# Performance work log

Hardware: AMD Instinct MI355X
Metric: run time of the kernel (lower is better)

The kernel has to match this reference:

```python
import jax, jax.numpy as jnp
import numpy as np

N = 50000
E = 1600000
INPUT_DIM = 128
HEADS = 4
OUT_DIM = 32
LRELU_ALPHA = 0.2


def setup_inputs() -> dict:
    key = jax.random.key(0)
    k1, k2, k3, k4, k5 = jax.random.split(key, 5)
    gain = 1.0 / (1.0 + LRELU_ALPHA)
    input_proj = jax.random.normal(k1, (N, INPUT_DIM), dtype=jnp.float32)
    edge_index = jax.random.randint(k2, (2, E), 0, N, dtype=jnp.int64)
    W = jax.random.normal(k3, (INPUT_DIM, HEADS * OUT_DIM), dtype=jnp.float32) * (gain / INPUT_DIM) ** 0.5
    A_left = jax.random.normal(k4, (HEADS, OUT_DIM, 1), dtype=jnp.float32) * (gain / OUT_DIM)
    A_right = jax.random.normal(k5, (HEADS, OUT_DIM, 1), dtype=jnp.float32) * (gain / OUT_DIM)
    return {"input_proj": input_proj, "edge_index": edge_index, "W": W, "A_left": A_left, "A_right": A_right}


def reference(input_proj, edge_index, W, A_left, A_right):
    n = input_proj.shape[0]
    heads, out_dim = A_left.shape[0], A_left.shape[1]
    # Linear projection: [N, heads, out_dim]
    H = (input_proj @ W).reshape(n, heads, out_dim)
    # Per-node attention scores: [N, heads]
    H_s = jnp.einsum('nhd,hd->nh', H, A_left[..., 0])
    H_t = jnp.einsum('nhd,hd->nh', H, A_right[..., 0])
    src = edge_index[0]
    tgt = edge_index[1]
    # Edge scores: leaky_relu(H_s[src] + H_t[tgt]) -> [E, heads]
    e = H_s[src] + H_t[tgt]
    e = jnp.where(e > 0, e, LRELU_ALPHA * e)
    # Segment softmax over neighborhoods keyed by source node (global max shift, as in original)
    e = jnp.exp(e - jnp.max(e))
    denom = jax.ops.segment_sum(e, src, num_segments=n)  # [N, heads]
    alpha = e / (denom[src] + 1e-8)
    # Weighted scatter-add aggregation of target features: [N, heads, out_dim]
    msg = alpha[:, :, None] * H[tgt]
    agg = jax.ops.segment_sum(msg, src, num_segments=n)
    # concat_last=True -> [N, heads*out_dim], then ELU
    res = agg.reshape(n, heads * out_dim)
    return jax.nn.elu(res)
```

## Files before the change

### kernel.cpp

```cpp
#include <hip/hip_runtime.h>
#include <hip/hip_fp16.h>

#define DIM 128
#define HEADS 4
#define ODIM 32
#define LRELU 0.2f
#define PT 4096
#define CAP 9216

typedef unsigned int u32;
typedef unsigned short u16;
typedef unsigned char u8;

typedef __attribute__((ext_vector_type(8))) short bf16x8;
typedef __attribute__((ext_vector_type(4))) float f32x4;

__device__ __forceinline__ u16 f2bf(float f) {
    union { u32 u; float f; } x; x.f = f;
    u32 u = x.u;
    u32 r = u + 0x7FFFu + ((u >> 16) & 1u);
    return (u16)(r >> 16);
}
__device__ __forceinline__ u32 pack_h2(float x, float y) {
    union { __half2 h; u32 u; } c;
    c.h = __floats2half2_rn(x, y);
    return c.u;
}
__device__ __forceinline__ float2 up2(u32 b) {
    union { u32 u; __half2 h; } c; c.u = b;
    return __half22float2(c.h);
}

__device__ __forceinline__ int scan256_excl(int v, int t, int* wsum) {
    int lane = t & 63, w = t >> 6;
    int inc = v;
    #pragma unroll
    for (int ofs = 1; ofs < 64; ofs <<= 1) {
        int x = __shfl_up(inc, ofs);
        if (lane >= ofs) inc += x;
    }
    __syncthreads();
    if (lane == 63) wsum[w] = inc;
    __syncthreads();
    int add = 0;
    #pragma unroll
    for (int j = 0; j < 4; ++j) add += (j < w) ? wsum[j] : 0;
    return inc - v + add;
}

__global__ __launch_bounds__(256) void prep_kernel(
    const float* __restrict__ W, u16* __restrict__ Wt, int* __restrict__ bcur)
{
    __shared__ u16 s[128 * 17];
    const int t = threadIdx.x;
    const int b = blockIdx.x;
    if (b == 0) bcur[t] = t * CAP;
    #pragma unroll
    for (int i = 0; i < 8; ++i) {
        int idx = i * 256 + t;
        int kk = idx >> 7;
        int nn = idx & 127;
        s[nn * 17 + kk] = f2bf(W[(b * 16 + kk) * 128 + nn]);
    }
    __syncthreads();
    #pragma unroll
    for (int i = 0; i < 8; ++i) {
        int idx = i * 256 + t;
        int nn = idx >> 4;
        int kk = idx & 15;
        Wt[nn * 128 + b * 16 + kk] = s[nn * 17 + kk];
    }
}

__device__ __forceinline__ void partition_body(
    char* smem, int bid, const int* __restrict__ ei, int* __restrict__ bcur,
    u32* __restrict__ part, int E, int n)
{
    u32* stage = (u32*)smem;
    u8*  sbkt  = (u8*)(smem + 16384);
    int (*lcnt4)[256] = (int (*)[256])(smem + 20480);
    int (*lcur4)[256] = (int (*)[256])(smem + 24576);
    int* loff  = (int*)(smem + 28672);
    int* ltot  = (int*)(smem + 29696);
    int* gbase = (int*)(smem + 30720);
    int* wsum  = (int*)(smem + 31744);
    const int t = threadIdx.x;
    const int wv = t >> 6;
    const int base = bid * PT;
    lcnt4[0][t] = 0; lcnt4[1][t] = 0; lcnt4[2][t] = 0; lcnt4[3][t] = 0;
    __syncthreads();

    int srcv[16], tgtv[16];
    #pragma unroll
    for (int i = 0; i < 16; ++i) {
        int e = base + i * 256 + t;
        srcv[i] = (e < E) ? ei[e] : -1;
    }
    #pragma unroll
    for (int i = 0; i < 16; ++i) {
        int e = base + i * 256 + t;
        tgtv[i] = (e < E) ? ei[E + e] : 0;
    }
    u32 key[16];
    int bkt[16];
    #pragma unroll
    for (int i = 0; i < 16; ++i) {
        bkt[i] = -1;
        key[i] = 0;
        if (srcv[i] >= 0) {
            int src = min(srcv[i], n - 1);
            int tgt = max(0, min(tgtv[i], n - 1));
            bkt[i] = src >> 8;
            key[i] = ((u32)(src & 255) << 17) | (u32)tgt;
        }
    }
    #pragma unroll
    for (int i = 0; i < 16; ++i)
        if (bkt[i] >= 0) atomicAdd(&lcnt4[wv][bkt[i]], 1);
    __syncthreads();
    int c0 = lcnt4[0][t], c1 = lcnt4[1][t], c2 = lcnt4[2][t], c3 = lcnt4[3][t];
    int total = c0 + c1 + c2 + c3;
    int ex = scan256_excl(total, t, wsum);
    loff[t] = ex;
    ltot[t] = total;
    lcur4[0][t] = ex;
    lcur4[1][t] = ex + c0;
    lcur4[2][t] = ex + c0 + c1;
    lcur4[3][t] = ex + c0 + c1 + c2;
    gbase[t] = (total > 0) ? atomicAdd(&bcur[t], total) : 0;
    __syncthreads();
    #pragma unroll
    for (int i = 0; i < 16; ++i) {
        if (bkt[i] >= 0) {
            int p = atomicAdd(&lcur4[wv][bkt[i]], 1);
            stage[p] = key[i];
            sbkt[p] = (u8)bkt[i];
        }
    }
    __syncthreads();
    int tot = loff[255] + ltot[255];
    for (int i = t; i < tot; i += 256) {
        int b = sbkt[i];
        int dst = gbase[b] + (i - loff[b]);
        if (dst < (b + 1) * CAP) part[dst] = stage[i];
    }
}

__device__ __forceinline__ void proj_body(
    char* smem, int bid, const float* __restrict__ X, const u16* __restrict__ Wt,
    const float* __restrict__ AL, const float* __restrict__ AR,
    u32* __restrict__ Hb, float* __restrict__ Hs, float* __restrict__ Ht, int n)
{
    float* sH  = (float*)smem;
    float* sAL = (float*)(smem + 33792);
    float* sAR = (float*)(smem + 34304);
    const int t = threadIdx.x;
    if (t < DIM) { sAL[t] = AL[t]; sAR[t] = AR[t]; }
    const int row0 = bid * 64;
    const int w = t >> 6, lane = t & 63;
    const int quad = lane >> 4, nIdx = lane & 15;
    const int m = row0 + w * 16 + nIdx;

    f32x4 acc[8];
    #pragma unroll
    for (int c = 0; c < 8; ++c) acc[c] = (f32x4){0.f, 0.f, 0.f, 0.f};

    #pragma unroll
    for (int kq = 0; kq < 4; ++kq) {
        union { bf16x8 v; u16 e[8]; } a;
        if (m < n) {
            const float* xp = &X[(size_t)m * DIM + kq * 32 + quad * 8];
            float4 x0 = *(const float4*)xp;
            float4 x1 = *(const float4*)(xp + 4);
            a.e[0] = f2bf(x0.x); a.e[1] = f2bf(x0.y);
            a.e[2] = f2bf(x0.z); a.e[3] = f2bf(x0.w);
            a.e[4] = f2bf(x1.x); a.e[5] = f2bf(x1.y);
            a.e[6] = f2bf(x1.z); a.e[7] = f2bf(x1.w);
        } else {
            #pragma unroll
            for (int j = 0; j < 8; ++j) a.e[j] = 0;
        }
        #pragma unroll
        for (int c = 0; c < 8; ++c) {
            bf16x8 b = *(const bf16x8*)&Wt[(c * 16 + nIdx) * DIM + kq * 32 + quad * 8];
            acc[c] = __builtin_amdgcn_mfma_f32_16x16x32_bf16(a.v, b, acc[c], 0, 0, 0);
        }
    }
    #pragma unroll
    for (int c = 0; c < 8; ++c)
        #pragma unroll
        for (int r = 0; r < 4; ++r)
            sH[(w * 16 + quad * 4 + r) * 132 + c * 16 + nIdx] = acc[c][r];
    __syncthreads();

    #pragma unroll
    for (int i = 0; i < 16; ++i) {
        int idx = i * 256 + t;
        int r = idx >> 6, d2 = idx & 63;
        int gr = row0 + r;
        if (gr < n) {
            float2 hv = *(const float2*)&sH[r * 132 + 2 * d2];
            Hb[(size_t)gr * 64 + d2] = pack_h2(hv.x, hv.y);
        }
    }
    {
        int r = t >> 2, h = t & 3;
        float s = 0.f, s2 = 0.f;
        #pragma unroll
        for (int q = 0; q < ODIM; q += 4) {
            float4 hv = *(const float4*)&sH[r * 132 + h * ODIM + q];
            s  += hv.x*sAL[h*ODIM+q] + hv.y*sAL[h*ODIM+q+1] + hv.z*sAL[h*ODIM+q+2] + hv.w*sAL[h*ODIM+q+3];
            s2 += hv.x*sAR[h*ODIM+q] + hv.y*sAR[h*ODIM+q+1] + hv.z*sAR[h*ODIM+q+2] + hv.w*sAR[h*ODIM+q+3];
        }
        int gr = row0 + r;
        if (gr < n) { Hs[gr * HEADS + h] = s; Ht[gr * HEADS + h] = s2; }
    }
}

__global__ __launch_bounds__(256) void fused_pp_kernel(
    const float* __restrict__ X, const u16* __restrict__ Wt,
    const float* __restrict__ AL, const float* __restrict__ AR,
    u32* __restrict__ Hb, float* __restrict__ Hs, float* __restrict__ Ht,
    const int* __restrict__ ei, int* __restrict__ bcur, u32* __restrict__ part,
    int n, int E, int partBlocks)
{
    __shared__ alignas(16) char smem[34816];
    if ((int)blockIdx.x < partBlocks)
        partition_body(smem, blockIdx.x, ei, bcur, part, E, n);
    else
        proj_body(smem, blockIdx.x - partBlocks, X, Wt, AL, AR, Hb, Hs, Ht, n);
}

__global__ __launch_bounds__(256) void csrfill_kernel(
    const u32* __restrict__ part, const int* __restrict__ bcur,
    int* __restrict__ off, int* __restrict__ csr_tgt, int n, int ntiles)
{
    __shared__ u32 skey[CAP];
    __shared__ int lc4[4][128];
    __shared__ int lcur4[4][128];
    __shared__ int wsum[4];
    __shared__ int sBase, sCnt;
    const int blk = blockIdx.x, t = threadIdx.x;
    const int b = blk >> 1, half = blk & 1;
    const int wv = t >> 6;
    int myc = (t < ntiles) ? (bcur[t] - t * CAP) : 0;
    myc = max(0, min(myc, CAP));
    int ex = scan256_excl(myc, t, wsum);
    if (t == b) { sBase = ex; sCnt = myc; }
    if (t < 128) { lc4[0][t] = 0; lc4[1][t] = 0; lc4[2][t] = 0; lc4[3][t] = 0; }
    __syncthreads();
    const int pbase = b * CAP;
    const int base = sBase, cnt = sCnt;
    for (int i = t; i < cnt; i += 1024) {
        u32 k[4];
        #pragma unroll
        for (int u = 0; u < 4; ++u) {
            int idx = i + u * 256;
            k[u] = (idx < cnt) ? part[pbase + idx] : 0xFFFFFFFFu;
        }
        #pragma unroll
        for (int u = 0; u < 4; ++u) {
            int idx = i + u * 256;
            if (idx < cnt) skey[idx] = k[u];
            int n8 = (int)(k[u] >> 17);
            if ((n8 >> 7) == half) atomicAdd(&lc4[wv][n8 & 127], 1);
        }
    }
    __syncthreads();
    int c0 = 0, c1 = 0, c2 = 0, c3 = 0, total = 0;
    if (t < 128) {
        c0 = lc4[0][t]; c1 = lc4[1][t]; c2 = lc4[2][t]; c3 = lc4[3][t];
        total = c0 + c1 + c2 + c3;
    }
    int ex2 = scan256_excl(total, t, wsum);
    int halfTot = wsum[0] + wsum[1];
    int myBase = base + (half ? (cnt - halfTot) : 0);
    if (t < 128) {
        lcur4[0][t] = ex2;
        lcur4[1][t] = ex2 + c0;
        lcur4[2][t] = ex2 + c0 + c1;
        lcur4[3][t] = ex2 + c0 + c1 + c2;
        int node = b * 256 + half * 128 + t;
        if (node < n) off[node] = myBase + ex2;
    }
    if (b == ntiles - 1 && half == 0 && t == 0) off[n] = base + cnt;
    __syncthreads();
    for (int i = t; i < cnt; i += 256) {
        u32 key = skey[i];
        int n8 = (int)(key >> 17);
        if ((n8 >> 7) == half) {
            int p = atomicAdd(&lcur4[wv][n8 & 127], 1);
            csr_tgt[myBase + p] = (int)(key & 0x1FFFFu);
        }
    }
}

__global__ __launch_bounds__(256) void agg_kernel(
    const u32* __restrict__ Hb, const float* __restrict__ Hs,
    const float* __restrict__ Ht, const int* __restrict__ off,
    const int* __restrict__ csr_tgt, float2* __restrict__ out, int n, int E)
{
    int node = (blockIdx.x * 256 + threadIdx.x) >> 6;
    int L = threadIdx.x & 63;
    if (node >= n) return;
    int lo = off[node], hi = off[node + 1];
    lo = max(0, min(lo, E));
    hi = max(lo, min(hi, E));
    if (hi <= lo) {
        out[(size_t)node * 64 + L] = {0.f, 0.f};
        return;
    }
    const int h = L >> 4;
    const int jSel = L >> 2;
    const int hSel = L & 3;
    float4 hs4 = *(const float4*)&Hs[node * HEADS];
    float hsD = hSel == 0 ? hs4.x : hSel == 1 ? hs4.y : hSel == 2 ? hs4.z : hs4.w;
    float ax = 0.f, ay = 0.f, Sd = 0.f;

    int tl = csr_tgt[min(lo + (L & 31), hi - 1)];
    for (int i = lo; i < hi; i += 32) {
        int tln = 0;
        if (i + 32 < hi) tln = csr_tgt[min(i + 32 + (L & 31), hi - 1)];
        int tA = __shfl(tl, jSel);
        int tB = __shfl(tl, jSel + 16);
        float eA = hsD + Ht[tA * HEADS + hSel];
        float eB = hsD + Ht[tB * HEADS + hSel];
        float wA = (i + jSel < hi)
                       ? __expf(fminf(eA > 0.f ? eA : LRELU * eA, 30.f)) : 0.f;
        float wB = (i + jSel + 16 < hi)
                       ? __expf(fminf(eB > 0.f ? eB : LRELU * eB, 30.f)) : 0.f;
        Sd += wA + wB;
        u32 bb[32];
        #pragma unroll
        for (int j = 0; j < 32; ++j) {
            int sj = __builtin_amdgcn_readlane(tl, j);
            bb[j] = Hb[((size_t)(u32)sj << 6) + L];
        }
        #pragma unroll
        for (int j = 0; j < 16; ++j) {
            float wj = __shfl(wA, (j << 2) | h);
            float2 f = up2(bb[j]);
            ax += wj * f.x;
            ay += wj * f.y;
        }
        #pragma unroll
        for (int j = 0; j < 16; ++j) {
            float wj = __shfl(wB, (j << 2) | h);
            float2 f = up2(bb[j + 16]);
            ax += wj * f.x;
            ay += wj * f.y;
        }
        tl = tln;
    }
    float S = 0.f;
    #pragma unroll
    for (int j = 0; j < 16; ++j) S += __shfl(Sd, (j << 2) | h);
    float inv = 1.f / (S + 1e-8f);
    float ox = ax * inv, oy = ay * inv;
    ox = ox > 0.f ? ox : (__expf(ox) - 1.f);
    oy = oy > 0.f ? oy : (__expf(oy) - 1.f);
    out[(size_t)node * 64 + L] = {ox, oy};
}

extern "C" void kernel_launch(void* const* d_in, const int* in_sizes, int n_in,
                              void* d_out, int out_size, void* d_ws, size_t ws_size,
                              hipStream_t stream) {
    const float* X  = (const float*)d_in[0];
    const int*   EI = (const int*)d_in[1];
    const float* W  = (const float*)d_in[2];
    const float* AL = (const float*)d_in[3];
    const float* AR = (const float*)d_in[4];
    const int n = in_sizes[0] / DIM;
    const int E = in_sizes[1] / 2;
    const int ntiles = (n + 255) / 256;

    char* ws = (char*)d_ws;
    size_t o = 0;
    auto alloc = [&](size_t bytes) -> void* {
        o = (o + 255) & ~(size_t)255;
        void* p = ws + o;
        o += bytes;
        return p;
    };
    int*   bcur    = (int*)alloc(256 * 4);
    u16*   Wt      = (u16*)alloc((size_t)DIM * DIM * 2);
    int*   off     = (int*)alloc((size_t)(n + 1) * 4);
    float* Hs      = (float*)alloc((size_t)n * HEADS * 4);
    float* Ht      = (float*)alloc((size_t)n * HEADS * 4);
    int*   csr_tgt = (int*)alloc((size_t)E * 4);
    u32*   part    = (u32*)alloc((size_t)ntiles * CAP * 4);
    u32*   Hb      = (u32*)alloc((size_t)n * 64 * 4);

    const int PB = (E + PT - 1) / PT;
    const int JB = (n + 63) / 64;

    prep_kernel<<<8, 256, 0, stream>>>(W, Wt, bcur);
    fused_pp_kernel<<<PB + JB, 256, 0, stream>>>(
        X, Wt, AL, AR, Hb, Hs, Ht, EI, bcur, part, n, E, PB);
    csrfill_kernel<<<ntiles * 2, 256, 0, stream>>>(part, bcur, off, csr_tgt, n, ntiles);
    agg_kernel<<<(n + 3) / 4, 256, 0, stream>>>(
        Hb, Hs, Ht, off, csr_tgt, (float2*)d_out, n, E);
}
```

Measured before the change: 184.5 us.

## Regroup kernels: fuse W prep with partition, fuse CSR fill with projection

Moves the W transpose into the same launch as edge partitioning, and runs the CSR fill alongside the node projection, which no longer depends on partitioning. The bucket cursor is now zeroed with a memset and holds relative counts. The CSR fill drops its 36KB shared staging buffer and rereads the partition from global memory on its second pass, which lowers shared memory per block so more blocks fit and co-schedule with projection blocks. The intent is to remove one dependent launch and overlap the independent projection with the CSR build, at the cost of an extra global read of the partition and a memset call.

```diff
diff --git a/kernel.cpp b/kernel.cpp
--- a/kernel.cpp
+++ b/kernel.cpp
@@ -48,13 +48,11 @@
     return inc - v + add;
 }
 
-__global__ __launch_bounds__(256) void prep_kernel(
-    const float* __restrict__ W, u16* __restrict__ Wt, int* __restrict__ bcur)
-{
-    __shared__ u16 s[128 * 17];
+__device__ __forceinline__ void wtprep_body(
+    char* smem, int b, const float* __restrict__ W, u16* __restrict__ Wt)
+{
+    u16* s = (u16*)smem;
     const int t = threadIdx.x;
-    const int b = blockIdx.x;
-    if (b == 0) bcur[t] = t * CAP;
     #pragma unroll
     for (int i = 0; i < 8; ++i) {
         int idx = i * 256 + t;
@@ -127,7 +125,8 @@
     lcur4[1][t] = ex + c0;
     lcur4[2][t] = ex + c0 + c1;
     lcur4[3][t] = ex + c0 + c1 + c2;
-    gbase[t] = (total > 0) ? atomicAdd(&bcur[t], total) : 0;
+    int gb = (total > 0) ? atomicAdd(&bcur[t], total) : 0;
+    gbase[t] = t * CAP + gb;
     __syncthreads();
     #pragma unroll
     for (int i = 0; i < 16; ++i) {
@@ -143,6 +142,89 @@
         int b = sbkt[i];
         int dst = gbase[b] + (i - loff[b]);
         if (dst < (b + 1) * CAP) part[dst] = stage[i];
+    }
+}
+
+__global__ __launch_bounds__(256) void fused_pw_kernel(
+    const float* __restrict__ W, u16* __restrict__ Wt,
+    const int* __restrict__ ei, int* __restrict__ bcur, u32* __restrict__ part,
+    int E, int n)
+{
+    __shared__ alignas(16) char smem[31760];
+    const int bid = (int)blockIdx.x;
+    if (bid < 8)
+        wtprep_body(smem, bid, W, Wt);
+    else
+        partition_body(smem, bid - 8, ei, bcur, part, E, n);
+}
+
+__device__ __forceinline__ void csrfill_body(
+    char* smem, int blk, const u32* __restrict__ part,
+    const int* __restrict__ bcur, int* __restrict__ off,
+    int* __restrict__ csr_tgt, int n, int ntiles)
+{
+    int (*lc4)[128]   = (int (*)[128])(smem);
+    int (*lcur4)[128] = (int (*)[128])(smem + 2048);
+    int* wsum = (int*)(smem + 4096);
+    int* sBC  = (int*)(smem + 4112);
+    const int t = threadIdx.x;
+    const int b = blk >> 1, half = blk & 1;
+    const int wv = t >> 6;
+    int myc = (t < ntiles) ? bcur[t] : 0;
+    myc = max(0, min(myc, CAP));
+    int ex = scan256_excl(myc, t, wsum);
+    if (t == b) { sBC[0] = ex; sBC[1] = myc; }
+    if (t < 128) { lc4[0][t] = 0; lc4[1][t] = 0; lc4[2][t] = 0; lc4[3][t] = 0; }
+    __syncthreads();
+    const int pbase = b * CAP;
+    const int base = sBC[0], cnt = sBC[1];
+    for (int i = t; i < cnt; i += 1024) {
+        u32 k[4];
+        #pragma unroll
+        for (int u = 0; u < 4; ++u) {
+            int idx = i + u * 256;
+            k[u] = (idx < cnt) ? part[pbase + idx] : 0xFFFFFFFFu;
+        }
+        #pragma unroll
+        for (int u = 0; u < 4; ++u) {
+            int n8 = (int)(k[u] >> 17);
+            if ((n8 >> 7) == half) atomicAdd(&lc4[wv][n8 & 127], 1);
+        }
+    }
+    __syncthreads();
+    int c0 = 0, c1 = 0, c2 = 0, c3 = 0, total = 0;
+    if (t < 128) {
+        c0 = lc4[0][t]; c1 = lc4[1][t]; c2 = lc4[2][t]; c3 = lc4[3][t];
+        total = c0 + c1 + c2 + c3;
+    }
+    int ex2 = scan256_excl(total, t, wsum);
+    int halfTot = wsum[0] + wsum[1];
+    int myBase = base + (half ? (cnt - halfTot) : 0);
+    if (t < 128) {
+        lcur4[0][t] = ex2;
+        lcur4[1][t] = ex2 + c0;
+        lcur4[2][t] = ex2 + c0 + c1;
+        lcur4[3][t] = ex2 + c0 + c1 + c2;
+        int node = b * 256 + half * 128 + t;
+        if (node < n) off[node] = myBase + ex2;
+    }
+    if (b == ntiles - 1 && half == 0 && t == 0) off[n] = base + cnt;
+    __syncthreads();
+    for (int i = t; i < cnt; i += 1024) {
+        u32 k[4];
+        #pragma unroll
+        for (int u = 0; u < 4; ++u) {
+            int idx = i + u * 256;
+            k[u] = (idx < cnt) ? part[pbase + idx] : 0xFFFFFFFFu;
+        }
+        #pragma unroll
+        for (int u = 0; u < 4; ++u) {
+            int n8 = (int)(k[u] >> 17);
+            if ((n8 >> 7) == half) {
+                int p = atomicAdd(&lcur4[wv][n8 & 127], 1);
+                csr_tgt[myBase + p] = (int)(k[u] & 0x1FFFFu);
+            }
+        }
     }
 }
 
@@ -217,82 +299,20 @@
     }
 }
 
-__global__ __launch_bounds__(256) void fused_pp_kernel(
+__global__ __launch_bounds__(256) void fused_cj_kernel(
     const float* __restrict__ X, const u16* __restrict__ Wt,
     const float* __restrict__ AL, const float* __restrict__ AR,
     u32* __restrict__ Hb, float* __restrict__ Hs, float* __restrict__ Ht,
-    const int* __restrict__ ei, int* __restrict__ bcur, u32* __restrict__ part,
-    int n, int E, int partBlocks)
+    const u32* __restrict__ part, const int* __restrict__ bcur,
+    int* __restrict__ off, int* __restrict__ csr_tgt,
+    int n, int ntiles, int csrBlocks)
 {
     __shared__ alignas(16) char smem[34816];
-    if ((int)blockIdx.x < partBlocks)
-        partition_body(smem, blockIdx.x, ei, bcur, part, E, n);
+    const int bid = (int)blockIdx.x;
+    if (bid < csrBlocks)
+        csrfill_body(smem, bid, part, bcur, off, csr_tgt, n, ntiles);
     else
-        proj_body(smem, blockIdx.x - partBlocks, X, Wt, AL, AR, Hb, Hs, Ht, n);
-}
-
-__global__ __launch_bounds__(256) void csrfill_kernel(
-    const u32* __restrict__ part, const int* __restrict__ bcur,
-    int* __restrict__ off, int* __restrict__ csr_tgt, int n, int ntiles)
-{
-    __shared__ u32 skey[CAP];
-    __shared__ int lc4[4][128];
-    __shared__ int lcur4[4][128];
-    __shared__ int wsum[4];
-    __shared__ int sBase, sCnt;
-    const int blk = blockIdx.x, t = threadIdx.x;
-    const int b = blk >> 1, half = blk & 1;
-    const int wv = t >> 6;
-    int myc = (t < ntiles) ? (bcur[t] - t * CAP) : 0;
-    myc = max(0, min(myc, CAP));
-    int ex = scan256_excl(myc, t, wsum);
-    if (t == b) { sBase = ex; sCnt = myc; }
-    if (t < 128) { lc4[0][t] = 0; lc4[1][t] = 0; lc4[2][t] = 0; lc4[3][t] = 0; }
-    __syncthreads();
-    const int pbase = b * CAP;
-    const int base = sBase, cnt = sCnt;
-    for (int i = t; i < cnt; i += 1024) {
-        u32 k[4];
-        #pragma unroll
-        for (int u = 0; u < 4; ++u) {
-            int idx = i + u * 256;
-            k[u] = (idx < cnt) ? part[pbase + idx] : 0xFFFFFFFFu;
-        }
-        #pragma unroll
-        for (int u = 0; u < 4; ++u) {
-            int idx = i + u * 256;
-            if (idx < cnt) skey[idx] = k[u];
-            int n8 = (int)(k[u] >> 17);
-            if ((n8 >> 7) == half) atomicAdd(&lc4[wv][n8 & 127], 1);
-        }
-    }
-    __syncthreads();
-    int c0 = 0, c1 = 0, c2 = 0, c3 = 0, total = 0;
-    if (t < 128) {
-        c0 = lc4[0][t]; c1 = lc4[1][t]; c2 = lc4[2][t]; c3 = lc4[3][t];
-        total = c0 + c1 + c2 + c3;
-    }
-    int ex2 = scan256_excl(total, t, wsum);
-    int halfTot = wsum[0] + wsum[1];
-    int myBase = base + (half ? (cnt - halfTot) : 0);
-    if (t < 128) {
-        lcur4[0][t] = ex2;
-        lcur4[1][t] = ex2 + c0;
-        lcur4[2][t] = ex2 + c0 + c1;
-        lcur4[3][t] = ex2 + c0 + c1 + c2;
-        int node = b * 256 + half * 128 + t;
-        if (node < n) off[node] = myBase + ex2;
-    }
-    if (b == ntiles - 1 && half == 0 && t == 0) off[n] = base + cnt;
-    __syncthreads();
-    for (int i = t; i < cnt; i += 256) {
-        u32 key = skey[i];
-        int n8 = (int)(key >> 17);
-        if ((n8 >> 7) == half) {
-            int p = atomicAdd(&lcur4[wv][n8 & 127], 1);
-            csr_tgt[myBase + p] = (int)(key & 0x1FFFFu);
-        }
-    }
+        proj_body(smem, bid - csrBlocks, X, Wt, AL, AR, Hb, Hs, Ht, n);
 }
 
 __global__ __launch_bounds__(256) void agg_kernel(
@@ -393,11 +413,12 @@
 
     const int PB = (E + PT - 1) / PT;
     const int JB = (n + 63) / 64;
-
-    prep_kernel<<<8, 256, 0, stream>>>(W, Wt, bcur);
-    fused_pp_kernel<<<PB + JB, 256, 0, stream>>>(
-        X, Wt, AL, AR, Hb, Hs, Ht, EI, bcur, part, n, E, PB);
-    csrfill_kernel<<<ntiles * 2, 256, 0, stream>>>(part, bcur, off, csr_tgt, n, ntiles);
+    const int CB = ntiles * 2;
+
+    hipMemsetAsync(bcur, 0, 256 * 4, stream);
+    fused_pw_kernel<<<8 + PB, 256, 0, stream>>>(W, Wt, EI, bcur, part, E, n);
+    fused_cj_kernel<<<CB + JB, 256, 0, stream>>>(
+        X, Wt, AL, AR, Hb, Hs, Ht, part, bcur, off, csr_tgt, n, ntiles, CB);
     agg_kernel<<<(n + 3) / 4, 256, 0, stream>>>(
         Hb, Hs, Ht, off, csr_tgt, (float2*)d_out, n, E);
 }
```

Measured after the change: 186.4 us. About the same (+1.0%).
